# Kernel tuning notes

Hardware: AMD Instinct MI355X
Metric: run time of the kernel (lower is better)

Reference implementation:

```python
import jax, jax.numpy as jnp
import numpy as np

B, S, D, H = 2, 2048, 768, 12
DK = D // H

def setup_inputs() -> dict:
    key = jax.random.key(0)
    ks = jax.random.split(key, 11)
    sc = 0.02
    inp = {
        'Q': jax.random.normal(ks[0], (B, S, D), jnp.float32),
        'K': jax.random.normal(ks[1], (B, S, D), jnp.float32),
        'V': jax.random.normal(ks[2], (B, S, D), jnp.float32),
        # causal mask, broadcastable over batch and heads (1 = keep, 0 = mask)
        'mask': jnp.tril(jnp.ones((S, S), jnp.int32))[None, None, :, :],
        'Wq': jax.random.normal(ks[3], (D, D), jnp.float32) * sc,
        'bq': jax.random.normal(ks[4], (D,), jnp.float32) * sc,
        'Wk': jax.random.normal(ks[5], (D, D), jnp.float32) * sc,
        'bk': jax.random.normal(ks[6], (D,), jnp.float32) * sc,
        'Wv': jax.random.normal(ks[7], (D, D), jnp.float32) * sc,
        'bv': jax.random.normal(ks[8], (D,), jnp.float32) * sc,
        'Wo': jax.random.normal(ks[9], (D, D), jnp.float32) * sc,
        'bo': jax.random.normal(ks[10], (D,), jnp.float32) * sc,
    }
    return inp

def _split_heads(x):
    # [B,S,D] -> [B,H,S,DK]
    return x.reshape(B, S, H, DK).transpose(0, 2, 1, 3)

def reference(Q, K, V, mask, Wq, bq, Wk, bk, Wv, bv, Wo, bo):
    # torch Linear: y = x @ W.T + b
    q = _split_heads(Q @ Wq.T + bq)
    k = _split_heads(K @ Wk.T + bk)
    v = _split_heads(V @ Wv.T + bv)
    scores = jnp.einsum('bhqd,bhkd->bhqk', q, k) / jnp.sqrt(jnp.float32(DK))
    scores = jnp.where(mask == 0, jnp.float32(-1e9), scores)
    attn = jax.nn.softmax(scores, axis=-1)
    out = jnp.einsum('bhqk,bhkd->bhqd', attn, v)  # [B,H,S,DK]
    out = out.transpose(0, 2, 1, 3).reshape(B, S, D)
    return out @ Wo.T + bo
```

## Files before the change

### kernel.cpp

```cpp
#include <hip/hip_runtime.h>
#include <hip/hip_bf16.h>

#define H_  12
#define S_  2048
#define D_  768
#define DK_ 64

typedef __bf16 bf16x8 __attribute__((ext_vector_type(8)));
typedef __bf16 bf16x4 __attribute__((ext_vector_type(4)));
typedef short  short4v __attribute__((ext_vector_type(4)));
typedef float  f32x4  __attribute__((ext_vector_type(4)));

#define QSCALE 0.1803368801111137f

__device__ inline float exp2_fast(float x) {
  return __builtin_amdgcn_exp2f(x);
}

__device__ inline f32x4 mfma_bf16(bf16x8 a, bf16x8 b, f32x4 c) {
  return __builtin_amdgcn_mfma_f32_16x16x32_bf16(a, b, c, 0, 0, 0);
}

__device__ inline f32x4 mfma16(bf16x4 a, bf16x4 b, f32x4 c) {
#if __has_builtin(__builtin_amdgcn_mfma_f32_16x16x16bf16_1k)
  short4v as = __builtin_bit_cast(short4v, a);
  short4v bs = __builtin_bit_cast(short4v, b);
  return __builtin_amdgcn_mfma_f32_16x16x16bf16_1k(as, bs, c, 0, 0, 0);
#else
  asm("s_nop 1\n\tv_mfma_f32_16x16x16_bf16 %0, %1, %2, %0"
      : "+v"(c) : "v"(a), "v"(b));
  return c;
#endif
}

__device__ inline void gload16(const void* g, void* l) {
  __builtin_amdgcn_global_load_lds(
      (const __attribute__((address_space(1))) void*)g,
      (__attribute__((address_space(3))) void*)l, 16, 0, 0);
}

__device__ inline bf16x8 cvt2bf16(f32x4 a, f32x4 b) {
  bf16x8 r;
  r[0] = (__bf16)a[0]; r[1] = (__bf16)a[1];
  r[2] = (__bf16)a[2]; r[3] = (__bf16)a[3];
  r[4] = (__bf16)b[0]; r[5] = (__bf16)b[1];
  r[6] = (__bf16)b[2]; r[7] = (__bf16)b[3];
  return r;
}

__global__ __launch_bounds__(256)
void conv_w(const float* __restrict__ Wq, const float* __restrict__ Wk,
            const float* __restrict__ Wv, const float* __restrict__ Wo,
            __hip_bfloat16* __restrict__ out)
{
  const int i8 = blockIdx.x * 256 + threadIdx.x;
  const int mat = i8 / 73728;
  const int off = (i8 - mat * 73728) * 8;
  const float* src = (mat == 0) ? Wq : (mat == 1) ? Wk : (mat == 2) ? Wv : Wo;
  f32x4 a = *(const f32x4*)(src + off);
  f32x4 b = *(const f32x4*)(src + off + 4);
  *(bf16x8*)(out + (size_t)mat * 589824 + off) = cvt2bf16(a, b);
}

__global__ __launch_bounds__(256, 3)
void qkv_proj(const float* __restrict__ Q, const float* __restrict__ K,
              const float* __restrict__ V,
              const __hip_bfloat16* __restrict__ Wb,
              const float* __restrict__ bq, const float* __restrict__ bk,
              const float* __restrict__ bv,
              __hip_bfloat16* __restrict__ q_ws,
              __hip_bfloat16* __restrict__ k_ws,
              __hip_bfloat16* __restrict__ vT_ws)
{
  __shared__ alignas(16) __hip_bfloat16 Ald[128 * 32];
  __shared__ alignas(16) __hip_bfloat16 Bld[128 * 32];

  const int z = blockIdx.z;
  const float* X    = (z == 0) ? Q  : (z == 1) ? K  : V;
  const float* bias = (z == 0) ? bq : (z == 1) ? bk : bv;
  const __hip_bfloat16* Wz = Wb + (size_t)z * 589824;
  __hip_bfloat16* out = (z == 0) ? q_ws : (z == 1) ? k_ws : vT_ws;
  const bool vmode = (z == 2);
  const float osc = (z == 0) ? QSCALE : 1.0f;

  const int t    = threadIdx.x;
  const int w    = t >> 6;
  const int lane = t & 63;
  const int l15  = lane & 15;
  const int quad = lane >> 4;
  const int m0 = blockIdx.x * 128;
  const int n0 = blockIdx.y * 128;
  const int wm = (w >> 1) * 64;
  const int wn = (w & 1) * 64;

  __hip_bfloat16* Xbuf = vmode ? Bld : Ald;
  __hip_bfloat16* Wbuf = vmode ? Ald : Bld;

  const f32x4 fzero = {0.f, 0.f, 0.f, 0.f};
  f32x4 acc[4][4];
#pragma unroll
  for (int i = 0; i < 4; ++i)
#pragma unroll
    for (int j = 0; j < 4; ++j) acc[i][j] = fzero;

  const int ar = t >> 2, ac = t & 3;
  const int sw = ac ^ ((ar >> 1) & 3);
  const float* As0 = X + (size_t)(m0 + ar) * D_ + ac * 8;
  const float* As1 = X + (size_t)(m0 + ar + 64) * D_ + ac * 8;
  __hip_bfloat16* Xw0 = &Xbuf[((ar)      * 4 + sw) * 8];
  __hip_bfloat16* Xw1 = &Xbuf[((ar + 64) * 4 + sw) * 8];

  const int bp = (t & 3) ^ (((t >> 2) >> 1) & 3);
  const __hip_bfloat16* Bs0 = Wz + (size_t)(n0 + (t >> 2)) * D_ + bp * 8;
  const __hip_bfloat16* Bs1 = Wz + (size_t)(n0 + (t >> 2) + 64) * D_ + bp * 8;
  __hip_bfloat16* Wd0 = &Wbuf[t * 8];
  __hip_bfloat16* Wd1 = &Wbuf[(t + 256) * 8];

  int agrn[4], bgrn[4];
#pragma unroll
  for (int i = 0; i < 4; ++i) {
    int row = wm + 16 * i + l15;
    agrn[i] = (row * 4 + (quad ^ ((row >> 1) & 3))) * 8;
    row = wn + 16 * i + l15;
    bgrn[i] = (row * 4 + (quad ^ ((row >> 1) & 3))) * 8;
  }

  f32x4 a00 = *(const f32x4*)As0, a01 = *(const f32x4*)(As0 + 4);
  f32x4 a10 = *(const f32x4*)As1, a11 = *(const f32x4*)(As1 + 4);

  for (int k0 = 0; k0 < D_; k0 += 32) {
    *(bf16x8*)Xw0 = cvt2bf16(a00, a01);
    *(bf16x8*)Xw1 = cvt2bf16(a10, a11);
    gload16(Bs0 + k0, Wd0);
    gload16(Bs1 + k0, Wd1);
    __syncthreads();

    const int kn = k0 + 32;
    if (kn < D_) {
      a00 = *(const f32x4*)(As0 + kn); a01 = *(const f32x4*)(As0 + kn + 4);
      a10 = *(const f32x4*)(As1 + kn); a11 = *(const f32x4*)(As1 + kn + 4);
    }

    bf16x8 af[4], bfr[4];
#pragma unroll
    for (int i = 0; i < 4; ++i) af[i]  = *(const bf16x8*)&Ald[agrn[i]];
#pragma unroll
    for (int j = 0; j < 4; ++j) bfr[j] = *(const bf16x8*)&Bld[bgrn[j]];
#pragma unroll
    for (int i = 0; i < 4; ++i)
#pragma unroll
      for (int j = 0; j < 4; ++j)
        acc[i][j] = mfma_bf16(af[i], bfr[j], acc[i][j]);
    __syncthreads();
  }

  if (!vmode) {
#pragma unroll
    for (int j = 0; j < 4; ++j) {
      const int n_g = n0 + wn + 16 * j + l15;
      const float bv = bias[n_g];
      const int hh = n_g >> 6, dk = n_g & (DK_ - 1);
#pragma unroll
      for (int i = 0; i < 4; ++i) {
        const int mbase = m0 + wm + 16 * i + quad * 4;
#pragma unroll
        for (int r = 0; r < 4; ++r) {
          const int m_g = mbase + r;
          const int bb = m_g >> 11, ss = m_g & (S_ - 1);
          const float vout = (acc[i][j][r] + bv) * osc;
          out[(((size_t)(bb * H_ + hh)) * S_ + ss) * DK_ + dk] =
              __float2bfloat16(vout);
        }
      }
    }
  } else {
#pragma unroll
    for (int i = 0; i < 4; ++i) {
      const int nbase = n0 + wm + 16 * i + quad * 4;
#pragma unroll
      for (int r = 0; r < 4; ++r) {
        const int n_g = nbase + r;
        const float bv = bias[n_g];
        const int hh = n_g >> 6, dk = n_g & (DK_ - 1);
#pragma unroll
        for (int j = 0; j < 4; ++j) {
          const int m_g = m0 + wn + 16 * j + l15;
          const int bb = m_g >> 11, ss = m_g & (S_ - 1);
          out[(((size_t)(bb * H_ + hh)) * DK_ + dk) * S_ + ss] =
              __float2bfloat16(acc[i][j][r] + bv);
        }
      }
    }
  }
}

__global__ __launch_bounds__(256, 4)
void o_proj(const __hip_bfloat16* __restrict__ Xb,
            const __hip_bfloat16* __restrict__ Wob,
            const float* __restrict__ bias,
            float* __restrict__ outf)
{
  __shared__ alignas(16) __hip_bfloat16 Ald[64 * 32];
  __shared__ alignas(16) __hip_bfloat16 Bld[128 * 32];

  const int t    = threadIdx.x;
  const int w    = t >> 6;
  const int lane = t & 63;
  const int l15  = lane & 15;
  const int quad = lane >> 4;
  const int m0 = blockIdx.x * 64;
  const int n0 = blockIdx.y * 128;
  const int wm = (w >> 1) * 32;
  const int wn = (w & 1) * 64;

  const f32x4 fzero = {0.f, 0.f, 0.f, 0.f};
  f32x4 acc[2][4];
#pragma unroll
  for (int i = 0; i < 2; ++i)
#pragma unroll
    for (int j = 0; j < 4; ++j) acc[i][j] = fzero;

  const int ap = (t & 3) ^ (((t >> 2) >> 1) & 3);
  const __hip_bfloat16* As  = Xb  + (size_t)(m0 + (t >> 2)) * D_ + ap * 8;
  const __hip_bfloat16* Bs0 = Wob + (size_t)(n0 + (t >> 2)) * D_ + ap * 8;
  const __hip_bfloat16* Bs1 = Wob + (size_t)(n0 + (t >> 2) + 64) * D_ + ap * 8;
  __hip_bfloat16* Ad  = &Ald[t * 8];
  __hip_bfloat16* Bd0 = &Bld[t * 8];
  __hip_bfloat16* Bd1 = &Bld[(t + 256) * 8];

  int agrn[2], bgrn[4];
#pragma unroll
  for (int i = 0; i < 2; ++i) {
    const int row = wm + 16 * i + l15;
    agrn[i] = (row * 4 + (quad ^ ((row >> 1) & 3))) * 8;
  }
#pragma unroll
  for (int j = 0; j < 4; ++j) {
    const int row = wn + 16 * j + l15;
    bgrn[j] = (row * 4 + (quad ^ ((row >> 1) & 3))) * 8;
  }

  for (int k0 = 0; k0 < D_; k0 += 32) {
    gload16(As + k0, Ad);
    gload16(Bs0 + k0, Bd0);
    gload16(Bs1 + k0, Bd1);
    __syncthreads();

    bf16x8 af[2], bfr[4];
#pragma unroll
    for (int i = 0; i < 2; ++i) af[i]  = *(const bf16x8*)&Ald[agrn[i]];
#pragma unroll
    for (int j = 0; j < 4; ++j) bfr[j] = *(const bf16x8*)&Bld[bgrn[j]];
#pragma unroll
    for (int i = 0; i < 2; ++i)
#pragma unroll
      for (int j = 0; j < 4; ++j)
        acc[i][j] = mfma_bf16(af[i], bfr[j], acc[i][j]);
    __syncthreads();
  }

#pragma unroll
  for (int j = 0; j < 4; ++j) {
    const int n_g = n0 + wn + 16 * j + l15;
    const float bv = bias[n_g];
#pragma unroll
    for (int i = 0; i < 2; ++i) {
      const int mbase = m0 + wm + 16 * i + quad * 4;
#pragma unroll
      for (int r = 0; r < 4; ++r)
        outf[(size_t)(mbase + r) * D_ + n_g] = acc[i][j][r] + bv;
    }
  }
}

__global__ __launch_bounds__(256, 4)
void flash_attn(const __hip_bfloat16* __restrict__ q_ws,
                const __hip_bfloat16* __restrict__ k_ws,
                const __hip_bfloat16* __restrict__ vT_ws,
                __hip_bfloat16* __restrict__ o_ws)
{
  __shared__ alignas(16) __hip_bfloat16 Kld[128][72];
  __shared__ alignas(16) __hip_bfloat16 Vld[64][136];

  const int t = threadIdx.x, w = t >> 6, lane = t & 63;
  const int l15 = lane & 15, quad = lane >> 4;

  const int id   = blockIdx.x;
  const int slot = id & 7;
  const int jj   = id >> 3;
  const int grp  = jj >> 5;
  const int bh   = slot + 8 * grp;
  const int x    = ((jj & 31) + 13 * grp) & 31;

  const int b = bh / H_, h = bh % H_;
  const int tLo = x, tHi = 63 - x;
  const int myTile = (w < 2) ? tLo : tHi;
  const int qbase = myTile * 32 + 16 * (w & 1);
  const int qg = qbase + l15;
  const int myNkt = (myTile >> 2) + 1;
  const int nktT  = (tHi >> 2) + 1;
  const size_t hbase = (size_t)bh * S_ * DK_;
  const size_t vtb   = (size_t)bh * DK_ * S_;

  bf16x8 qf[2];
#pragma unroll
  for (int kk = 0; kk < 2; ++kk)
    qf[kk] = *(const bf16x8*)(q_ws + hbase + (size_t)qg * DK_ + kk * 32 + quad * 8);

  const f32x4 fzero = {0.f, 0.f, 0.f, 0.f};
  f32x4 accO[4];
#pragma unroll
  for (int jd = 0; jd < 4; ++jd) accO[jd] = fzero;
  float mI = -1.0e30f, lI = 0.f;

  const int tr = t >> 3, kg = t & 7;
  const int tv = t >> 4, vg = t & 15;
  const __hip_bfloat16* Kbase = k_ws + hbase + (size_t)tr * DK_ + kg * 8;
  const __hip_bfloat16* Vbase = vT_ws + vtb + (size_t)tv * S_ + vg * 8;

  bf16x8 rK[4], rV[4];
#pragma unroll
  for (int it = 0; it < 4; ++it) {
    rK[it] = *(const bf16x8*)(Kbase + (size_t)(32 * it) * DK_);
    rV[it] = *(const bf16x8*)(Vbase + (size_t)(16 * it) * S_);
  }

  for (int kt = 0; kt < nktT; ++kt) {
#pragma unroll
    for (int it = 0; it < 4; ++it) {
      *(bf16x8*)&Kld[32 * it + tr][kg * 8] = rK[it];
      *(bf16x8*)&Vld[16 * it + tv][vg * 8] = rV[it];
    }
    __syncthreads();

    if (kt + 1 < nktT) {
      const int k0n = (kt + 1) * 128;
#pragma unroll
      for (int it = 0; it < 4; ++it) {
        rK[it] = *(const bf16x8*)(Kbase + (size_t)(k0n + 32 * it) * DK_);
        rV[it] = *(const bf16x8*)(Vbase + (size_t)(16 * it) * S_ + k0n);
      }
    }

    if (kt < myNkt) {
      const int k0 = kt * 128;
      f32x4 st[8];
#pragma unroll
      for (int j = 0; j < 8; ++j) {
        bf16x8 kf0 = *(const bf16x8*)&Kld[16 * j + l15][quad * 8];
        bf16x8 kf1 = *(const bf16x8*)&Kld[16 * j + l15][32 + quad * 8];
        st[j] = mfma_bf16(kf0, qf[0], fzero);
        st[j] = mfma_bf16(kf1, qf[1], st[j]);
      }

      if (kt == myNkt - 1) {
#pragma unroll
        for (int j = 0; j < 8; ++j)
#pragma unroll
          for (int r = 0; r < 4; ++r) {
            const int kcg = k0 + 16 * j + quad * 4 + r;
            if (kcg > qg) st[j][r] = -1.0e9f;
          }
      }

      float tm = st[0][0];
#pragma unroll
      for (int j = 0; j < 8; ++j)
#pragma unroll
        for (int r = 0; r < 4; ++r) tm = fmaxf(tm, st[j][r]);
      tm = fmaxf(tm, __shfl_xor(tm, 16));
      tm = fmaxf(tm, __shfl_xor(tm, 32));

      const float mnew = fmaxf(mI, tm);
      const float al = exp2_fast(mI - mnew);
      mI = mnew;
      float rs = 0.f;
#pragma unroll
      for (int j = 0; j < 8; ++j)
#pragma unroll
        for (int r = 0; r < 4; ++r) {
          const float pv = exp2_fast(st[j][r] - mnew);
          st[j][r] = pv;
          rs += pv;
        }
      rs += __shfl_xor(rs, 16);
      rs += __shfl_xor(rs, 32);
      lI = lI * al + rs;
#pragma unroll
      for (int jd = 0; jd < 4; ++jd)
#pragma unroll
        for (int r = 0; r < 4; ++r) accO[jd][r] *= al;

      bf16x4 pb[8];
#pragma unroll
      for (int j = 0; j < 8; ++j) {
        pb[j][0] = (__bf16)st[j][0]; pb[j][1] = (__bf16)st[j][1];
        pb[j][2] = (__bf16)st[j][2]; pb[j][3] = (__bf16)st[j][3];
      }

#pragma unroll
      for (int jd = 0; jd < 4; ++jd)
#pragma unroll
        for (int j = 0; j < 8; ++j) {
          bf16x4 vf = *(const bf16x4*)&Vld[16 * jd + l15][16 * j + quad * 4];
          accO[jd] = mfma16(vf, pb[j], accO[jd]);
        }
    }
    __syncthreads();
  }

  const float inv = 1.f / lI;
#pragma unroll
  for (int jd = 0; jd < 4; ++jd) {
    bf16x4 ov;
#pragma unroll
    for (int r = 0; r < 4; ++r) ov[r] = (__bf16)(accO[jd][r] * inv);
    *(bf16x4*)(o_ws + ((size_t)b * S_ + qg) * D_ + h * DK_ + 16 * jd + quad * 4) = ov;
  }
}

extern "C" void kernel_launch(void* const* d_in, const int* in_sizes, int n_in,
                              void* d_out, int out_size, void* d_ws, size_t ws_size,
                              hipStream_t stream) {
  (void)in_sizes; (void)n_in; (void)out_size; (void)ws_size;
  const float* Q  = (const float*)d_in[0];
  const float* K  = (const float*)d_in[1];
  const float* V  = (const float*)d_in[2];
  const float* Wq = (const float*)d_in[4];
  const float* bq = (const float*)d_in[5];
  const float* Wk = (const float*)d_in[6];
  const float* bk = (const float*)d_in[7];
  const float* Wv = (const float*)d_in[8];
  const float* bv = (const float*)d_in[9];
  const float* Wo = (const float*)d_in[10];
  const float* bo = (const float*)d_in[11];
  float* out = (float*)d_out;

  const size_t WEL = (size_t)4 * 589824;
  const size_t NEL = (size_t)2 * S_ * D_;
  __hip_bfloat16* wb    = (__hip_bfloat16*)d_ws;
  __hip_bfloat16* q_ws  = wb + WEL;
  __hip_bfloat16* k_ws  = q_ws  + NEL;
  __hip_bfloat16* vT_ws = k_ws  + NEL;
  __hip_bfloat16* o_ws  = vT_ws + NEL;

  conv_w<<<1152, 256, 0, stream>>>(Wq, Wk, Wv, Wo, wb);
  qkv_proj<<<dim3(32, 6, 3), 256, 0, stream>>>(Q, K, V, wb, bq, bk, bv,
                                               q_ws, k_ws, vT_ws);
  flash_attn<<<768, 256, 0, stream>>>(q_ws, k_ws, vT_ws, o_ws);
  o_proj<<<dim3(64, 6), 256, 0, stream>>>(o_ws, wb + (size_t)3 * 589824, bo, out);
}
```

Before: 193.2 us.

## Split attention KV range across two blocks and merge partials before output projection

Flash attention now launches twice as many blocks. Each block handles alternating 128-key tiles for one half, then writes unnormalized partial outputs and per-row max/sum stats. A new merge kernel combines the two partials with log-sum-exp weights, and o_proj reads the head-major partial layout with a smaller 64x64 tile and twice the grid. This is meant to raise occupancy and parallelism on the attention stage. In exchange it adds an extra kernel launch, extra global traffic for partials, and bf16 rounding of the unnormalized accumulators.

```diff
diff --git a/kernel.cpp b/kernel.cpp
--- a/kernel.cpp
+++ b/kernel.cpp
@@ -195,89 +195,12 @@
 }
 
 __global__ __launch_bounds__(256, 4)
-void o_proj(const __hip_bfloat16* __restrict__ Xb,
-            const __hip_bfloat16* __restrict__ Wob,
-            const float* __restrict__ bias,
-            float* __restrict__ outf)
-{
-  __shared__ alignas(16) __hip_bfloat16 Ald[64 * 32];
-  __shared__ alignas(16) __hip_bfloat16 Bld[128 * 32];
-
-  const int t    = threadIdx.x;
-  const int w    = t >> 6;
-  const int lane = t & 63;
-  const int l15  = lane & 15;
-  const int quad = lane >> 4;
-  const int m0 = blockIdx.x * 64;
-  const int n0 = blockIdx.y * 128;
-  const int wm = (w >> 1) * 32;
-  const int wn = (w & 1) * 64;
-
-  const f32x4 fzero = {0.f, 0.f, 0.f, 0.f};
-  f32x4 acc[2][4];
-#pragma unroll
-  for (int i = 0; i < 2; ++i)
-#pragma unroll
-    for (int j = 0; j < 4; ++j) acc[i][j] = fzero;
-
-  const int ap = (t & 3) ^ (((t >> 2) >> 1) & 3);
-  const __hip_bfloat16* As  = Xb  + (size_t)(m0 + (t >> 2)) * D_ + ap * 8;
-  const __hip_bfloat16* Bs0 = Wob + (size_t)(n0 + (t >> 2)) * D_ + ap * 8;
-  const __hip_bfloat16* Bs1 = Wob + (size_t)(n0 + (t >> 2) + 64) * D_ + ap * 8;
-  __hip_bfloat16* Ad  = &Ald[t * 8];
-  __hip_bfloat16* Bd0 = &Bld[t * 8];
-  __hip_bfloat16* Bd1 = &Bld[(t + 256) * 8];
-
-  int agrn[2], bgrn[4];
-#pragma unroll
-  for (int i = 0; i < 2; ++i) {
-    const int row = wm + 16 * i + l15;
-    agrn[i] = (row * 4 + (quad ^ ((row >> 1) & 3))) * 8;
-  }
-#pragma unroll
-  for (int j = 0; j < 4; ++j) {
-    const int row = wn + 16 * j + l15;
-    bgrn[j] = (row * 4 + (quad ^ ((row >> 1) & 3))) * 8;
-  }
-
-  for (int k0 = 0; k0 < D_; k0 += 32) {
-    gload16(As + k0, Ad);
-    gload16(Bs0 + k0, Bd0);
-    gload16(Bs1 + k0, Bd1);
-    __syncthreads();
-
-    bf16x8 af[2], bfr[4];
-#pragma unroll
-    for (int i = 0; i < 2; ++i) af[i]  = *(const bf16x8*)&Ald[agrn[i]];
-#pragma unroll
-    for (int j = 0; j < 4; ++j) bfr[j] = *(const bf16x8*)&Bld[bgrn[j]];
-#pragma unroll
-    for (int i = 0; i < 2; ++i)
-#pragma unroll
-      for (int j = 0; j < 4; ++j)
-        acc[i][j] = mfma_bf16(af[i], bfr[j], acc[i][j]);
-    __syncthreads();
-  }
-
-#pragma unroll
-  for (int j = 0; j < 4; ++j) {
-    const int n_g = n0 + wn + 16 * j + l15;
-    const float bv = bias[n_g];
-#pragma unroll
-    for (int i = 0; i < 2; ++i) {
-      const int mbase = m0 + wm + 16 * i + quad * 4;
-#pragma unroll
-      for (int r = 0; r < 4; ++r)
-        outf[(size_t)(mbase + r) * D_ + n_g] = acc[i][j][r] + bv;
-    }
-  }
-}
-
-__global__ __launch_bounds__(256, 4)
 void flash_attn(const __hip_bfloat16* __restrict__ q_ws,
                 const __hip_bfloat16* __restrict__ k_ws,
                 const __hip_bfloat16* __restrict__ vT_ws,
-                __hip_bfloat16* __restrict__ o_ws)
+                __hip_bfloat16* __restrict__ Op0,
+                __hip_bfloat16* __restrict__ Op1,
+                float2* __restrict__ mlbuf)
 {
   __shared__ alignas(16) __hip_bfloat16 Kld[128][72];
   __shared__ alignas(16) __hip_bfloat16 Vld[64][136];
@@ -289,10 +212,10 @@
   const int slot = id & 7;
   const int jj   = id >> 3;
   const int grp  = jj >> 5;
-  const int bh   = slot + 8 * grp;
+  const int bh   = slot + 8 * (grp % 3);
+  const int half = grp / 3;
   const int x    = ((jj & 31) + 13 * grp) & 31;
 
-  const int b = bh / H_, h = bh % H_;
   const int tLo = x, tHi = 63 - x;
   const int myTile = (w < 2) ? tLo : tHi;
   const int qbase = myTile * 32 + 16 * (w & 1);
@@ -319,13 +242,14 @@
   const __hip_bfloat16* Vbase = vT_ws + vtb + (size_t)tv * S_ + vg * 8;
 
   bf16x8 rK[4], rV[4];
+  const int k0h = half * 128;
 #pragma unroll
   for (int it = 0; it < 4; ++it) {
-    rK[it] = *(const bf16x8*)(Kbase + (size_t)(32 * it) * DK_);
-    rV[it] = *(const bf16x8*)(Vbase + (size_t)(16 * it) * S_);
-  }
-
-  for (int kt = 0; kt < nktT; ++kt) {
+    rK[it] = *(const bf16x8*)(Kbase + (size_t)(k0h + 32 * it) * DK_);
+    rV[it] = *(const bf16x8*)(Vbase + (size_t)(16 * it) * S_ + k0h);
+  }
+
+  for (int kt = half; kt < nktT; kt += 2) {
 #pragma unroll
     for (int it = 0; it < 4; ++it) {
       *(bf16x8*)&Kld[32 * it + tr][kg * 8] = rK[it];
@@ -333,8 +257,8 @@
     }
     __syncthreads();
 
-    if (kt + 1 < nktT) {
-      const int k0n = (kt + 1) * 128;
+    if (kt + 2 < nktT) {
+      const int k0n = (kt + 2) * 128;
 #pragma unroll
       for (int it = 0; it < 4; ++it) {
         rK[it] = *(const bf16x8*)(Kbase + (size_t)(k0n + 32 * it) * DK_);
@@ -409,13 +333,123 @@
     __syncthreads();
   }
 
-  const float inv = 1.f / lI;
+  __hip_bfloat16* Obase = half ? Op1 : Op0;
 #pragma unroll
   for (int jd = 0; jd < 4; ++jd) {
     bf16x4 ov;
 #pragma unroll
-    for (int r = 0; r < 4; ++r) ov[r] = (__bf16)(accO[jd][r] * inv);
-    *(bf16x4*)(o_ws + ((size_t)b * S_ + qg) * D_ + h * DK_ + 16 * jd + quad * 4) = ov;
+    for (int r = 0; r < 4; ++r) ov[r] = (__bf16)accO[jd][r];
+    *(bf16x4*)(Obase + ((size_t)bh * S_ + qg) * 64 + 16 * jd + quad * 4) = ov;
+  }
+  if (quad == 0) {
+    float2 v; v.x = mI; v.y = lI;
+    mlbuf[(size_t)(half * 24 + bh) * S_ + qg] = v;
+  }
+}
+
+__global__ __launch_bounds__(256)
+void fa_merge(__hip_bfloat16* __restrict__ Op0,
+              const __hip_bfloat16* __restrict__ Op1,
+              const float2* __restrict__ ml)
+{
+  const int tid = blockIdx.x * 256 + threadIdx.x;
+  const int row = tid >> 3;
+  const int d8  = tid & 7;
+  const float2 ml0 = ml[row];
+  const float2 ml1 = ml[24 * S_ + row];
+  const float m  = fmaxf(ml0.x, ml1.x);
+  const float w0 = exp2_fast(ml0.x - m);
+  const float w1 = exp2_fast(ml1.x - m);
+  const float inv = 1.f / (ml0.y * w0 + ml1.y * w1);
+  const float f0 = w0 * inv, f1 = w1 * inv;
+  const size_t base = (size_t)row * 64 + d8 * 8;
+  bf16x8 a = *(const bf16x8*)(Op0 + base);
+  bf16x8 b = *(const bf16x8*)(Op1 + base);
+  bf16x8 o;
+#pragma unroll
+  for (int i = 0; i < 8; ++i)
+    o[i] = (__bf16)((float)a[i] * f0 + (float)b[i] * f1);
+  *(bf16x8*)(Op0 + base) = o;
+}
+
+__global__ __launch_bounds__(256, 4)
+void o_proj(const __hip_bfloat16* __restrict__ Xp,
+            const __hip_bfloat16* __restrict__ Wob,
+            const float* __restrict__ bias,
+            float* __restrict__ outf)
+{
+  __shared__ alignas(16) __hip_bfloat16 Ald[64 * 32];
+  __shared__ alignas(16) __hip_bfloat16 Bld[64 * 32];
+
+  const int t    = threadIdx.x;
+  const int w    = t >> 6;
+  const int lane = t & 63;
+  const int l15  = lane & 15;
+  const int quad = lane >> 4;
+  const int m0 = blockIdx.x * 64;
+  const int n0 = blockIdx.y * 64;
+  const int wm = (w >> 1) * 32;
+  const int wn = (w & 1) * 32;
+
+  const f32x4 fzero = {0.f, 0.f, 0.f, 0.f};
+  f32x4 acc[2][2];
+#pragma unroll
+  for (int i = 0; i < 2; ++i)
+#pragma unroll
+    for (int j = 0; j < 2; ++j) acc[i][j] = fzero;
+
+  const int arow = t >> 2;
+  const int asw  = (t & 3) ^ ((arow >> 1) & 3);
+  const int m_g  = m0 + arow;
+  const int ab   = m_g >> 11, as = m_g & (S_ - 1);
+  const size_t arowbase = ((size_t)ab * H_) * S_ * 64 + (size_t)as * 64;
+
+  const int bsw = asw;
+  const __hip_bfloat16* Bs = Wob + (size_t)(n0 + arow) * D_ + bsw * 8;
+  __hip_bfloat16* Ad = &Ald[t * 8];
+  __hip_bfloat16* Bd = &Bld[t * 8];
+
+  int agrn[2], bgrn[2];
+#pragma unroll
+  for (int i = 0; i < 2; ++i) {
+    int row = wm + 16 * i + l15;
+    agrn[i] = (row * 4 + (quad ^ ((row >> 1) & 3))) * 8;
+    row = wn + 16 * i + l15;
+    bgrn[i] = (row * 4 + (quad ^ ((row >> 1) & 3))) * 8;
+  }
+
+  for (int k0 = 0; k0 < D_; k0 += 32) {
+    const int cg = (k0 >> 3) + asw;
+    const __hip_bfloat16* Ap =
+        Xp + arowbase + (size_t)(cg >> 3) * (S_ * 64) + (cg & 7) * 8;
+    gload16(Ap, Ad);
+    gload16(Bs + k0, Bd);
+    __syncthreads();
+
+    bf16x8 af[2], bfr[2];
+#pragma unroll
+    for (int i = 0; i < 2; ++i) af[i]  = *(const bf16x8*)&Ald[agrn[i]];
+#pragma unroll
+    for (int j = 0; j < 2; ++j) bfr[j] = *(const bf16x8*)&Bld[bgrn[j]];
+#pragma unroll
+    for (int i = 0; i < 2; ++i)
+#pragma unroll
+      for (int j = 0; j < 2; ++j)
+        acc[i][j] = mfma_bf16(af[i], bfr[j], acc[i][j]);
+    __syncthreads();
+  }
+
+#pragma unroll
+  for (int j = 0; j < 2; ++j) {
+    const int n_g = n0 + wn + 16 * j + l15;
+    const float bv = bias[n_g];
+#pragma unroll
+    for (int i = 0; i < 2; ++i) {
+      const int mbase = m0 + wm + 16 * i + quad * 4;
+#pragma unroll
+      for (int r = 0; r < 4; ++r)
+        outf[(size_t)(mbase + r) * D_ + n_g] = acc[i][j][r] + bv;
+    }
   }
 }
 
@@ -442,11 +476,14 @@
   __hip_bfloat16* q_ws  = wb + WEL;
   __hip_bfloat16* k_ws  = q_ws  + NEL;
   __hip_bfloat16* vT_ws = k_ws  + NEL;
-  __hip_bfloat16* o_ws  = vT_ws + NEL;
+  __hip_bfloat16* op0   = vT_ws + NEL;
+  __hip_bfloat16* op1   = op0   + NEL;
+  float2*         mlbuf = (float2*)(op1 + NEL);
 
   conv_w<<<1152, 256, 0, stream>>>(Wq, Wk, Wv, Wo, wb);
   qkv_proj<<<dim3(32, 6, 3), 256, 0, stream>>>(Q, K, V, wb, bq, bk, bv,
                                                q_ws, k_ws, vT_ws);
-  flash_attn<<<768, 256, 0, stream>>>(q_ws, k_ws, vT_ws, o_ws);
-  o_proj<<<dim3(64, 6), 256, 0, stream>>>(o_ws, wb + (size_t)3 * 589824, bo, out);
-}
+  flash_attn<<<1536, 256, 0, stream>>>(q_ws, k_ws, vT_ws, op0, op1, mlbuf);
+  fa_merge<<<1536, 256, 0, stream>>>(op0, op1, mlbuf);
+  o_proj<<<dim3(64, 12), 256, 0, stream>>>(op0, wb + (size_t)3 * 589824, bo, out);
+}
```

New measurement: 196.5 us. About the same (+1.8%).
